# Kernel tuning notes

Hardware: AMD Instinct MI355X
Metric: run time of the kernel (lower is better)

Reference implementation:

```python
import jax, jax.numpy as jnp
import numpy as np

N_HEAD, D_MODEL, D_K, D_V = 16, 1024, 64, 64
B, S = 4, 2048


def setup_inputs() -> dict:
    key = jax.random.key(0)
    ks = jax.random.split(key, 11)
    s = 0.02
    return {
        "q": jax.random.normal(ks[0], (B, S, D_MODEL), jnp.float32),
        "k": jax.random.normal(ks[1], (B, S, D_MODEL), jnp.float32),
        "v": jax.random.normal(ks[2], (B, S, D_MODEL), jnp.float32),
        "Wq": jax.random.normal(ks[3], (D_MODEL, N_HEAD * D_K), jnp.float32) * s,
        "bq": jnp.zeros((N_HEAD * D_K,), jnp.float32),
        "Wk": jax.random.normal(ks[4], (D_MODEL, N_HEAD * D_K), jnp.float32) * s,
        "bk": jnp.zeros((N_HEAD * D_K,), jnp.float32),
        "Wv": jax.random.normal(ks[5], (D_MODEL, N_HEAD * D_V), jnp.float32) * s,
        "bv": jnp.zeros((N_HEAD * D_V,), jnp.float32),
        "Wo": jax.random.normal(ks[6], (N_HEAD * D_V, D_MODEL), jnp.float32) * s,
        "bo": jnp.zeros((D_MODEL,), jnp.float32),
    }


def reference(q, k, v, Wq, bq, Wk, bk, Wv, bv, Wo, bo):
    b, s, _ = q.shape
    # project and split heads: [B,S,H,Dk] -> [B,H,S,Dk]
    qh = (q @ Wq + bq).reshape(b, s, N_HEAD, D_K).transpose(0, 2, 1, 3)
    kh = (k @ Wk + bk).reshape(b, s, N_HEAD, D_K).transpose(0, 2, 1, 3)
    vh = (v @ Wv + bv).reshape(b, s, N_HEAD, D_V).transpose(0, 2, 1, 3)
    scale = 1.0 / jnp.sqrt(jnp.float32(D_K))
    scores = jnp.einsum("bhqd,bhkd->bhqk", qh, kh) * scale  # [B,H,S,S]
    atten = jax.nn.softmax(scores, axis=-1)
    out = jnp.einsum("bhqk,bhkd->bhqd", atten, vh)  # [B,H,S,Dv]
    out = out.transpose(0, 2, 1, 3).reshape(b, s, N_HEAD * D_V)
    return out @ Wo + bo
```

## Files before the change

### kernel.cpp

```cpp
#include <hip/hip_runtime.h>

typedef unsigned short u16;
typedef __attribute__((ext_vector_type(4))) float f32x4;
typedef __attribute__((ext_vector_type(16))) float f32x16;
typedef __attribute__((ext_vector_type(8))) short bf16x8;
typedef __attribute__((ext_vector_type(4))) u16 u16x4;
typedef __attribute__((ext_vector_type(8))) u16 u16x8;

#define MFMA16(a, b, c) __builtin_amdgcn_mfma_f32_16x16x32_bf16((a), (b), (c), 0, 0, 0)
#define MFMA32(a, b, c) __builtin_amdgcn_mfma_f32_32x32x16_bf16((a), (b), (c), 0, 0, 0)

__device__ __forceinline__ u16 f2bf(float f) {
  union { float f; unsigned u; } x; x.f = f;
  unsigned r = x.u + 0x7fffu + ((x.u >> 16) & 1u);
  return (u16)(r >> 16);
}

__device__ __forceinline__ unsigned cvtpk(float lo, float hi) {
  unsigned r;
  asm("v_cvt_pk_bf16_f32 %0, %1, %2" : "=v"(r) : "v"(lo), "v"(hi));
  return r;
}

__device__ __forceinline__ void gl_lds16(const void* g, void* l) {
  __builtin_amdgcn_global_load_lds((const __attribute__((address_space(1))) void*)g,
                                   (__attribute__((address_space(3))) void*)l,
                                   16, 0, 0);
}

__global__ __launch_bounds__(256) void cvt3_k(const float* __restrict__ q, const float* __restrict__ k,
                                              const float* __restrict__ v, u16* __restrict__ dst, int n4) {
  const float* src = blockIdx.y == 0 ? q : (blockIdx.y == 1 ? k : v);
  u16* d = dst + (size_t)blockIdx.y * 8192 * 1024;
  int idx = blockIdx.x * blockDim.x + threadIdx.x;
  int stride = gridDim.x * blockDim.x;
  for (int i = idx; i < n4; i += stride) {
    float4 vv = ((const float4*)src)[i];
    u16x4 o;
    o[0] = f2bf(vv.x); o[1] = f2bf(vv.y); o[2] = f2bf(vv.z); o[3] = f2bf(vv.w);
    ((u16x4*)d)[i] = o;
  }
}

__global__ __launch_bounds__(256) void cvtT_k(const float* __restrict__ W0, const float* __restrict__ W1,
                                              const float* __restrict__ W2, const float* __restrict__ W3,
                                              u16* __restrict__ T0, u16* __restrict__ T1,
                                              u16* __restrict__ T2, u16* __restrict__ T3) {
  __shared__ u16 t[64][72];
  const float* W; u16* T;
  switch (blockIdx.z) {
    case 0: W = W0; T = T0; break;
    case 1: W = W1; T = T1; break;
    case 2: W = W2; T = T2; break;
    default: W = W3; T = T3; break;
  }
  const int tid = threadIdx.x;
  const int tr = blockIdx.x, tc = blockIdx.y;
#pragma unroll
  for (int i = 0; i < 4; ++i) {
    int row = i * 16 + (tid >> 4);
    int c4 = tid & 15;
    float4 v = *(const float4*)&W[(size_t)(tr * 64 + row) * 1024 + tc * 64 + c4 * 4];
    t[row][c4 * 4 + 0] = f2bf(v.x);
    t[row][c4 * 4 + 1] = f2bf(v.y);
    t[row][c4 * 4 + 2] = f2bf(v.z);
    t[row][c4 * 4 + 3] = f2bf(v.w);
  }
  __syncthreads();
#pragma unroll
  for (int i = 0; i < 4; ++i) {
    int orow = i * 16 + (tid >> 4);
    int occ = tid & 15;
    u16x4 o;
#pragma unroll
    for (int j = 0; j < 4; ++j) o[j] = t[occ * 4 + j][orow];
    *(u16x4*)&T[(size_t)(tc * 64 + orow) * 1024 + tr * 64 + occ * 4] = o;
  }
}

__global__ __launch_bounds__(256) void gemm_qkv_k(const u16* __restrict__ Xb, const u16* __restrict__ WTb,
                                                  const float* __restrict__ bq, const float* __restrict__ bk,
                                                  const float* __restrict__ bv,
                                                  u16* __restrict__ Qh, u16* __restrict__ Kh,
                                                  u16* __restrict__ Vt, float qscale) {
  __shared__ u16 As[128 * 64];
  __shared__ u16 Bs[128 * 64];
  const int tid = threadIdx.x;
  const int lane = tid & 63;
  const int w = tid >> 6;
  const int which = blockIdx.y >> 3;
  const int m0 = blockIdx.x * 128;
  const int n0 = (blockIdx.y & 7) * 128;
  const u16* X = Xb + (size_t)which * 8192 * 1024;
  const u16* WT = WTb + (size_t)which * 1024 * 1024;
  const float* bias = which == 0 ? bq : (which == 1 ? bk : bv);
  const int wr = (w >> 1) * 64;
  const int wc = (w & 1) * 64;
  const int srow = lane >> 3;
  const int sch = (lane & 7) * 8;
  f32x4 acc[4][4] = {};

  for (int ks = 0; ks < 16; ++ks) {
    const int k0 = ks * 64;
#pragma unroll
    for (int i = 0; i < 4; ++i) {
      int row = i * 32 + w * 8 + srow;
      gl_lds16(X + (size_t)(m0 + row) * 1024 + k0 + sch, &As[(i * 32 + w * 8) * 64]);
      gl_lds16(WT + (size_t)(n0 + row) * 1024 + k0 + sch, &Bs[(i * 32 + w * 8) * 64]);
    }
    __syncthreads();
#pragma unroll
    for (int kk = 0; kk < 2; ++kk) {
      bf16x8 a[4], b[4];
#pragma unroll
      for (int t = 0; t < 4; ++t) {
        a[t] = *(const bf16x8*)&As[(wr + t * 16 + (lane & 15)) * 64 + kk * 32 + (lane >> 4) * 8];
        b[t] = *(const bf16x8*)&Bs[(wc + t * 16 + (lane & 15)) * 64 + kk * 32 + (lane >> 4) * 8];
      }
#pragma unroll
      for (int mi = 0; mi < 4; ++mi)
#pragma unroll
        for (int ni = 0; ni < 4; ++ni)
          acc[mi][ni] = MFMA16(a[mi], b[ni], acc[mi][ni]);
    }
    __syncthreads();
  }

  const int lr = (lane >> 4) * 4;
  const int lc = lane & 15;
  if (which <= 1) {
    u16* ob = which == 0 ? Qh : Kh;
    float scale = which == 0 ? qscale : 1.0f;
#pragma unroll
    for (int mi = 0; mi < 4; ++mi)
#pragma unroll
      for (int ni = 0; ni < 4; ++ni) {
        int n = n0 + wc + ni * 16 + lc;
        float bb = bias[n];
        int h = n >> 6, d = n & 63;
#pragma unroll
        for (int r = 0; r < 4; ++r) {
          int m = m0 + wr + mi * 16 + lr + r;
          int b = m >> 11, s = m & 2047;
          ob[(((size_t)(b * 16 + h) * 2048 + s) << 6) + d] = f2bf((acc[mi][ni][r] + bb) * scale);
        }
      }
  } else {
#pragma unroll
    for (int mi = 0; mi < 4; ++mi)
#pragma unroll
      for (int ni = 0; ni < 4; ++ni) {
        int n = n0 + wc + ni * 16 + lc;
        float bb = bias[n];
        int h = n >> 6, d = n & 63;
        int m = m0 + wr + mi * 16 + lr;
        int b = m >> 11, s = m & 2047;
        u16x4 pk;
#pragma unroll
        for (int r = 0; r < 4; ++r) pk[r] = f2bf(acc[mi][ni][r] + bb);
        *(u16x4*)&Vt[((size_t)(b * 16 + h) * 64 + d) * 2048 + s] = pk;
      }
  }
}

__global__ __launch_bounds__(256) void gemm_o_k(const u16* __restrict__ X, const u16* __restrict__ WT,
                                                const float* __restrict__ bias, float* __restrict__ out) {
  __shared__ u16 As[128 * 64];
  __shared__ u16 Bs[128 * 64];
  const int tid = threadIdx.x;
  const int lane = tid & 63;
  const int w = tid >> 6;
  const int m0 = blockIdx.x * 128;
  const int n0 = blockIdx.y * 128;
  const int wr = (w >> 1) * 64;
  const int wc = (w & 1) * 64;
  const int srow = lane >> 3;
  const int sch = (lane & 7) * 8;
  f32x4 acc[4][4] = {};

  for (int ks = 0; ks < 16; ++ks) {
    const int k0 = ks * 64;
#pragma unroll
    for (int i = 0; i < 4; ++i) {
      int row = i * 32 + w * 8 + srow;
      gl_lds16(X + (size_t)(m0 + row) * 1024 + k0 + sch, &As[(i * 32 + w * 8) * 64]);
      gl_lds16(WT + (size_t)(n0 + row) * 1024 + k0 + sch, &Bs[(i * 32 + w * 8) * 64]);
    }
    __syncthreads();
#pragma unroll
    for (int kk = 0; kk < 2; ++kk) {
      bf16x8 a[4], b[4];
#pragma unroll
      for (int t = 0; t < 4; ++t) {
        a[t] = *(const bf16x8*)&As[(wr + t * 16 + (lane & 15)) * 64 + kk * 32 + (lane >> 4) * 8];
        b[t] = *(const bf16x8*)&Bs[(wc + t * 16 + (lane & 15)) * 64 + kk * 32 + (lane >> 4) * 8];
      }
#pragma unroll
      for (int mi = 0; mi < 4; ++mi)
#pragma unroll
        for (int ni = 0; ni < 4; ++ni)
          acc[mi][ni] = MFMA16(a[mi], b[ni], acc[mi][ni]);
    }
    __syncthreads();
  }

  const int lr = (lane >> 4) * 4;
  const int lc = lane & 15;
#pragma unroll
  for (int mi = 0; mi < 4; ++mi)
#pragma unroll
    for (int ni = 0; ni < 4; ++ni) {
      int n = n0 + wc + ni * 16 + lc;
      float bb = bias[n];
#pragma unroll
      for (int r = 0; r < 4; ++r) {
        int m = m0 + wr + mi * 16 + lr + r;
        out[(size_t)m * 1024 + n] = acc[mi][ni][r] + bb;
      }
    }
}

__global__ __launch_bounds__(512) void attn_k(const u16* __restrict__ Qh, const u16* __restrict__ Kh,
                                              const u16* __restrict__ Vt, u16* __restrict__ AO) {
  __shared__ u16 SMEM[6 * 4096];
  u16* KL = SMEM;
  u16* VL = SMEM + 3 * 4096;
  const int lane = threadIdx.x & 63, w = threadIdx.x >> 6;
  const int hi = lane >> 5, q = lane & 31;

  const int id = blockIdx.x;
  const int bh = ((id >> 3) & 7) * 8 + (id & 7);
  const int qt = id >> 6;
  const int q0 = qt * 256 + w * 32;

  const u16* Qb = Qh + (size_t)bh * 2048 * 64;
  const u16* Kb = Kh + (size_t)bh * 2048 * 64;
  const u16* Vb = Vt + (size_t)bh * 64 * 2048;

  bf16x8 qf[4];
#pragma unroll
  for (int c = 0; c < 4; ++c)
    qf[c] = *(const bf16x8*)&Qb[(size_t)(q0 + q) * 64 + c * 16 + hi * 8];

  f32x16 o0 = {}, o1 = {};
  float l_ = 0.f;

  const int skh = (w & 1) * 32;
  const int sck = ((w >> 1) * 2 + hi) * 8;
  const int srowK = skh + q;
  const int lo8 = lane * 8;

#define STAGE(buf_, kt_) do {                                                   \
    int k0_ = (kt_) * 64;                                                       \
    gl_lds16(Kb + (size_t)(k0_ + srowK) * 64 + sck, &KL[(buf_) * 4096 + w * 512]); \
    gl_lds16(Vb + (size_t)srowK * 2048 + k0_ + sck, &VL[(buf_) * 4096 + w * 512]); \
  } while (0)

  STAGE(0, 0);
  STAGE(1, 1);
  STAGE(2, 2);

  for (int kt = 0; kt < 32; ++kt) {
    if (kt < 30) asm volatile("s_waitcnt vmcnt(4)" ::: "memory");
    else         asm volatile("s_waitcnt vmcnt(0)" ::: "memory");
    __builtin_amdgcn_s_barrier();
    __builtin_amdgcn_sched_barrier(0);

    const u16* Kc = &KL[(kt % 3) * 4096];
    const u16* Vc = &VL[(kt % 3) * 4096];

    f32x16 s0 = {}, s1 = {};
    __builtin_amdgcn_s_setprio(1);
#pragma unroll
    for (int c = 0; c < 4; ++c) {
      bf16x8 k0 = *(const bf16x8*)&Kc[(c * 2) * 512 + lo8];
      bf16x8 k1 = *(const bf16x8*)&Kc[(c * 2 + 1) * 512 + lo8];
      s0 = MFMA32(k0, qf[c], s0);
      s1 = MFMA32(k1, qf[c], s1);
    }
    __builtin_amdgcn_s_setprio(0);

#pragma unroll
    for (int i = 0; i < 16; ++i) {
      s0[i] = __builtin_exp2f(s0[i]);
      s1[i] = __builtin_exp2f(s1[i]);
    }
    float sum = 0.f;
#pragma unroll
    for (int i = 0; i < 16; ++i) sum += s0[i] + s1[i];
    l_ += sum;

    __builtin_amdgcn_s_setprio(1);
#pragma unroll
    for (int t = 0; t < 4; ++t) {
      unsigned wA, wB, wC, wD;
      if (t == 0) { wA = cvtpk(s0[0], s0[1]); wB = cvtpk(s0[2], s0[3]); wC = cvtpk(s0[4], s0[5]); wD = cvtpk(s0[6], s0[7]); }
      else if (t == 1) { wA = cvtpk(s0[8], s0[9]); wB = cvtpk(s0[10], s0[11]); wC = cvtpk(s0[12], s0[13]); wD = cvtpk(s0[14], s0[15]); }
      else if (t == 2) { wA = cvtpk(s1[0], s1[1]); wB = cvtpk(s1[2], s1[3]); wC = cvtpk(s1[4], s1[5]); wD = cvtpk(s1[6], s1[7]); }
      else { wA = cvtpk(s1[8], s1[9]); wB = cvtpk(s1[10], s1[11]); wC = cvtpk(s1[12], s1[13]); wD = cvtpk(s1[14], s1[15]); }
      asm("v_permlane32_swap_b32 %0, %1" : "+v"(wA), "+v"(wC));
      asm("v_permlane32_swap_b32 %0, %1" : "+v"(wB), "+v"(wD));
      union { unsigned u[4]; bf16x8 v; } pf;
      pf.u[0] = wA; pf.u[1] = wB; pf.u[2] = wC; pf.u[3] = wD;
      bf16x8 v0 = *(const bf16x8*)&Vc[(t * 2) * 512 + lo8];
      bf16x8 v1 = *(const bf16x8*)&Vc[(t * 2 + 1) * 512 + lo8];
      o0 = MFMA32(v0, pf.v, o0);
      o1 = MFMA32(v1, pf.v, o1);
    }
    __builtin_amdgcn_s_setprio(0);

    __builtin_amdgcn_sched_barrier(0);
    __builtin_amdgcn_s_barrier();
    if (kt < 29) STAGE(kt % 3, kt + 3);
  }
#undef STAGE

  l_ += __shfl_xor(l_, 32);
  u16* ep = SMEM + w * 2048;
  float inv = 1.0f / l_;
#pragma unroll
  for (int g = 0; g < 2; ++g) {
    const f32x16 oo = g ? o1 : o0;
#pragma unroll
    for (int j = 0; j < 8; ++j) {
      int d = g * 32 + (j & 1) * 2 + ((j >> 1) & 1) * 8 + (j >> 2) * 16 + 4 * hi;
      unsigned pw = cvtpk(oo[2 * j] * inv, oo[2 * j + 1] * inv);
      *(unsigned*)&ep[q * 64 + ((d >> 3) ^ (q & 7)) * 8 + (d & 7)] = pw;
    }
  }
  asm volatile("s_waitcnt lgkmcnt(0)" ::: "memory");
  const int b = bh >> 4, h = bh & 15;
#pragma unroll
  for (int i = 0; i < 4; ++i) {
    int r = i * 8 + (lane >> 3), c = lane & 7;
    u16x8 vv = *(const u16x8*)&ep[r * 64 + ((c ^ (r & 7)) * 8)];
    size_t row = (size_t)b * 2048 + q0 + r;
    *(u16x8*)&AO[row * 1024 + h * 64 + c * 8] = vv;
  }
}

extern "C" void kernel_launch(void* const* d_in, const int* in_sizes, int n_in,
                              void* d_out, int out_size, void* d_ws, size_t ws_size,
                              hipStream_t stream) {
  const float* q  = (const float*)d_in[0];
  const float* k  = (const float*)d_in[1];
  const float* v  = (const float*)d_in[2];
  const float* Wq = (const float*)d_in[3];
  const float* bq = (const float*)d_in[4];
  const float* Wk = (const float*)d_in[5];
  const float* bk = (const float*)d_in[6];
  const float* Wv = (const float*)d_in[7];
  const float* bv = (const float*)d_in[8];
  const float* Wo = (const float*)d_in[9];
  const float* bo = (const float*)d_in[10];
  float* out = (float*)d_out;

  char* ws = (char*)d_ws;
  const size_t SZX = (size_t)8192 * 1024 * 2;
  const size_t SZW = (size_t)1024 * 1024 * 2;
  u16* Xq  = (u16*)(ws);
  u16* WTq = (u16*)(ws + 3 * SZX);
  u16* WTk = (u16*)(ws + 3 * SZX + SZW);
  u16* WTv = (u16*)(ws + 3 * SZX + 2 * SZW);
  u16* WTo = (u16*)(ws + 3 * SZX + 3 * SZW);
  u16* Qh  = (u16*)(ws + 3 * SZX + 4 * SZW);
  u16* Kh  = (u16*)(ws + 4 * SZX + 4 * SZW);
  u16* Vt  = (u16*)(ws + 5 * SZX + 4 * SZW);
  u16* AO  = Xq;

  const int n4 = 8192 * 1024 / 4;
  cvt3_k<<<dim3(1024, 3), dim3(256), 0, stream>>>(q, k, v, Xq, n4);
  cvtT_k<<<dim3(16, 16, 4), dim3(256), 0, stream>>>(Wq, Wk, Wv, Wo, WTq, WTk, WTv, WTo);

  gemm_qkv_k<<<dim3(64, 24), dim3(256), 0, stream>>>(Xq, WTq, bq, bk, bv, Qh, Kh, Vt,
                                                     0.125f * 1.4426950408889634f);

  attn_k<<<dim3(512), dim3(512), 0, stream>>>(Qh, Kh, Vt, AO);

  gemm_o_k<<<dim3(64, 8), dim3(256), 0, stream>>>(AO, WTo, bo, out);
}
```

Before: 227.8 us.

## Double-buffer 128-key tiles with one barrier per tile in attention

Replaces the triple-buffered 64-key K/V LDS pipeline with a double-buffered 128-key tile. Each iteration now waits for all loads, passes a single barrier, then issues the next tile's prefetch before computing. This halves the number of loop iterations and removes the second barrier per tile. It also swaps the block-to-(batch,head) index mapping, which changes L2 locality across blocks. The cost is less prefetch depth (vmcnt(0) every tile) and a larger LDS footprint of 64KB.

```diff
diff --git a/kernel.cpp b/kernel.cpp
--- a/kernel.cpp
+++ b/kernel.cpp
@@ -222,14 +222,12 @@
 
 __global__ __launch_bounds__(512) void attn_k(const u16* __restrict__ Qh, const u16* __restrict__ Kh,
                                               const u16* __restrict__ Vt, u16* __restrict__ AO) {
-  __shared__ u16 SMEM[6 * 4096];
-  u16* KL = SMEM;
-  u16* VL = SMEM + 3 * 4096;
+  __shared__ u16 SMEM[2 * 16384];
   const int lane = threadIdx.x & 63, w = threadIdx.x >> 6;
   const int hi = lane >> 5, q = lane & 31;
 
   const int id = blockIdx.x;
-  const int bh = ((id >> 3) & 7) * 8 + (id & 7);
+  const int bh = (id & 7) * 8 + ((id >> 3) & 7);
   const int qt = id >> 6;
   const int q0 = qt * 256 + w * 32;
 
@@ -244,76 +242,78 @@
 
   f32x16 o0 = {}, o1 = {};
   float l_ = 0.f;
-
-  const int skh = (w & 1) * 32;
-  const int sck = ((w >> 1) * 2 + hi) * 8;
-  const int srowK = skh + q;
   const int lo8 = lane * 8;
 
-#define STAGE(buf_, kt_) do {                                                   \
-    int k0_ = (kt_) * 64;                                                       \
-    gl_lds16(Kb + (size_t)(k0_ + srowK) * 64 + sck, &KL[(buf_) * 4096 + w * 512]); \
-    gl_lds16(Vb + (size_t)srowK * 2048 + k0_ + sck, &VL[(buf_) * 4096 + w * 512]); \
+#define STAGE(slot_, kt_) do {                                                        \
+    int k0_ = (kt_) * 128;                                                            \
+    u16* KS_ = SMEM + (slot_) * 16384;                                                \
+    u16* VS_ = KS_ + 8192;                                                            \
+    _Pragma("unroll")                                                                 \
+    for (int j_ = 0; j_ < 2; ++j_) {                                                  \
+      int f_ = 2 * w + j_;                                                            \
+      int kh_ = f_ >> 2, c_ = f_ & 3;                                                 \
+      gl_lds16(Kb + (size_t)(k0_ + kh_ * 32 + q) * 64 + (c_ * 2 + hi) * 8, KS_ + f_ * 512); \
+      gl_lds16(Vb + (size_t)(j_ * 32 + q) * 2048 + k0_ + (w * 2 + hi) * 8, VS_ + (w * 2 + j_) * 512); \
+    }                                                                                 \
   } while (0)
 
   STAGE(0, 0);
-  STAGE(1, 1);
-  STAGE(2, 2);
-
-  for (int kt = 0; kt < 32; ++kt) {
-    if (kt < 30) asm volatile("s_waitcnt vmcnt(4)" ::: "memory");
-    else         asm volatile("s_waitcnt vmcnt(0)" ::: "memory");
+
+  for (int kt = 0; kt < 16; ++kt) {
+    asm volatile("s_waitcnt vmcnt(0)" ::: "memory");
     __builtin_amdgcn_s_barrier();
+    if (kt < 15) STAGE((kt + 1) & 1, kt + 1);
     __builtin_amdgcn_sched_barrier(0);
 
-    const u16* Kc = &KL[(kt % 3) * 4096];
-    const u16* Vc = &VL[(kt % 3) * 4096];
-
-    f32x16 s0 = {}, s1 = {};
-    __builtin_amdgcn_s_setprio(1);
-#pragma unroll
-    for (int c = 0; c < 4; ++c) {
-      bf16x8 k0 = *(const bf16x8*)&Kc[(c * 2) * 512 + lo8];
-      bf16x8 k1 = *(const bf16x8*)&Kc[(c * 2 + 1) * 512 + lo8];
-      s0 = MFMA32(k0, qf[c], s0);
-      s1 = MFMA32(k1, qf[c], s1);
-    }
-    __builtin_amdgcn_s_setprio(0);
-
-#pragma unroll
-    for (int i = 0; i < 16; ++i) {
-      s0[i] = __builtin_exp2f(s0[i]);
-      s1[i] = __builtin_exp2f(s1[i]);
-    }
-    float sum = 0.f;
-#pragma unroll
-    for (int i = 0; i < 16; ++i) sum += s0[i] + s1[i];
-    l_ += sum;
-
-    __builtin_amdgcn_s_setprio(1);
-#pragma unroll
-    for (int t = 0; t < 4; ++t) {
-      unsigned wA, wB, wC, wD;
-      if (t == 0) { wA = cvtpk(s0[0], s0[1]); wB = cvtpk(s0[2], s0[3]); wC = cvtpk(s0[4], s0[5]); wD = cvtpk(s0[6], s0[7]); }
-      else if (t == 1) { wA = cvtpk(s0[8], s0[9]); wB = cvtpk(s0[10], s0[11]); wC = cvtpk(s0[12], s0[13]); wD = cvtpk(s0[14], s0[15]); }
-      else if (t == 2) { wA = cvtpk(s1[0], s1[1]); wB = cvtpk(s1[2], s1[3]); wC = cvtpk(s1[4], s1[5]); wD = cvtpk(s1[6], s1[7]); }
-      else { wA = cvtpk(s1[8], s1[9]); wB = cvtpk(s1[10], s1[11]); wC = cvtpk(s1[12], s1[13]); wD = cvtpk(s1[14], s1[15]); }
-      asm("v_permlane32_swap_b32 %0, %1" : "+v"(wA), "+v"(wC));
-      asm("v_permlane32_swap_b32 %0, %1" : "+v"(wB), "+v"(wD));
-      union { unsigned u[4]; bf16x8 v; } pf;
-      pf.u[0] = wA; pf.u[1] = wB; pf.u[2] = wC; pf.u[3] = wD;
-      bf16x8 v0 = *(const bf16x8*)&Vc[(t * 2) * 512 + lo8];
-      bf16x8 v1 = *(const bf16x8*)&Vc[(t * 2 + 1) * 512 + lo8];
-      o0 = MFMA32(v0, pf.v, o0);
-      o1 = MFMA32(v1, pf.v, o1);
-    }
-    __builtin_amdgcn_s_setprio(0);
-
-    __builtin_amdgcn_sched_barrier(0);
-    __builtin_amdgcn_s_barrier();
-    if (kt < 29) STAGE(kt % 3, kt + 3);
+    const u16* KS = SMEM + (kt & 1) * 16384;
+    const u16* VS = KS + 8192;
+
+#pragma unroll
+    for (int r = 0; r < 2; ++r) {
+      f32x16 s0 = {}, s1 = {};
+      __builtin_amdgcn_s_setprio(1);
+#pragma unroll
+      for (int c = 0; c < 4; ++c) {
+        bf16x8 k0 = *(const bf16x8*)&KS[((2 * r) * 4 + c) * 512 + lo8];
+        bf16x8 k1 = *(const bf16x8*)&KS[((2 * r + 1) * 4 + c) * 512 + lo8];
+        s0 = MFMA32(k0, qf[c], s0);
+        s1 = MFMA32(k1, qf[c], s1);
+      }
+      __builtin_amdgcn_s_setprio(0);
+
+#pragma unroll
+      for (int i = 0; i < 16; ++i) {
+        s0[i] = __builtin_exp2f(s0[i]);
+        s1[i] = __builtin_exp2f(s1[i]);
+      }
+      float sum = 0.f;
+#pragma unroll
+      for (int i = 0; i < 16; ++i) sum += s0[i] + s1[i];
+      l_ += sum;
+
+      __builtin_amdgcn_s_setprio(1);
+#pragma unroll
+      for (int t = 0; t < 4; ++t) {
+        unsigned wA, wB, wC, wD;
+        if (t == 0) { wA = cvtpk(s0[0], s0[1]); wB = cvtpk(s0[2], s0[3]); wC = cvtpk(s0[4], s0[5]); wD = cvtpk(s0[6], s0[7]); }
+        else if (t == 1) { wA = cvtpk(s0[8], s0[9]); wB = cvtpk(s0[10], s0[11]); wC = cvtpk(s0[12], s0[13]); wD = cvtpk(s0[14], s0[15]); }
+        else if (t == 2) { wA = cvtpk(s1[0], s1[1]); wB = cvtpk(s1[2], s1[3]); wC = cvtpk(s1[4], s1[5]); wD = cvtpk(s1[6], s1[7]); }
+        else { wA = cvtpk(s1[8], s1[9]); wB = cvtpk(s1[10], s1[11]); wC = cvtpk(s1[12], s1[13]); wD = cvtpk(s1[14], s1[15]); }
+        asm("v_permlane32_swap_b32 %0, %1" : "+v"(wA), "+v"(wC));
+        asm("v_permlane32_swap_b32 %0, %1" : "+v"(wB), "+v"(wD));
+        union { unsigned u[4]; bf16x8 v; } pf;
+        pf.u[0] = wA; pf.u[1] = wB; pf.u[2] = wC; pf.u[3] = wD;
+        bf16x8 v0 = *(const bf16x8*)&VS[((4 * r + t) * 2) * 512 + lo8];
+        bf16x8 v1 = *(const bf16x8*)&VS[((4 * r + t) * 2 + 1) * 512 + lo8];
+        o0 = MFMA32(v0, pf.v, o0);
+        o1 = MFMA32(v1, pf.v, o1);
+      }
+      __builtin_amdgcn_s_setprio(0);
+    }
   }
 #undef STAGE
+
+  __builtin_amdgcn_s_barrier();
 
   l_ += __shfl_xor(l_, 32);
   u16* ep = SMEM + w * 2048;
```

Result: slower. 238.5 us (+4.7%).

## Use four-slot LDS ring to drop second barrier, compute rowsum via MFMA

Applied to the files above, without the earlier changes.

The attention loop now uses a four-slot LDS ring instead of three, so the next tile can be issued right after the single per-iteration barrier. This removes the trailing barrier and lets the prefetch overlap the current tile's compute. The softmax denominator is now computed by an extra MFMA against a ones vector on the bf16 probabilities, replacing the scalar VALU sum and the cross-lane shuffle. The cost is 64KB of LDS instead of 48KB, one more MFMA per tile, and a denominator built from bf16-rounded probabilities.

```diff
diff --git a/kernel.cpp b/kernel.cpp
--- a/kernel.cpp
+++ b/kernel.cpp
@@ -222,9 +222,7 @@
 
 __global__ __launch_bounds__(512) void attn_k(const u16* __restrict__ Qh, const u16* __restrict__ Kh,
                                               const u16* __restrict__ Vt, u16* __restrict__ AO) {
-  __shared__ u16 SMEM[6 * 4096];
-  u16* KL = SMEM;
-  u16* VL = SMEM + 3 * 4096;
+  __shared__ u16 SMEM[4 * 8192];
   const int lane = threadIdx.x & 63, w = threadIdx.x >> 6;
   const int hi = lane >> 5, q = lane & 31;
 
@@ -242,18 +240,20 @@
   for (int c = 0; c < 4; ++c)
     qf[c] = *(const bf16x8*)&Qb[(size_t)(q0 + q) * 64 + c * 16 + hi * 8];
 
-  f32x16 o0 = {}, o1 = {};
-  float l_ = 0.f;
-
-  const int skh = (w & 1) * 32;
+  bf16x8 onesf;
+#pragma unroll
+  for (int i = 0; i < 8; ++i) onesf[i] = (short)0x3F80;
+
+  f32x16 o0 = {}, o1 = {}, ol = {};
+  const int lo8 = lane * 8;
+
+  const int srowK = (w & 1) * 32 + q;
   const int sck = ((w >> 1) * 2 + hi) * 8;
-  const int srowK = skh + q;
-  const int lo8 = lane * 8;
-
-#define STAGE(buf_, kt_) do {                                                   \
-    int k0_ = (kt_) * 64;                                                       \
-    gl_lds16(Kb + (size_t)(k0_ + srowK) * 64 + sck, &KL[(buf_) * 4096 + w * 512]); \
-    gl_lds16(Vb + (size_t)srowK * 2048 + k0_ + sck, &VL[(buf_) * 4096 + w * 512]); \
+
+#define STAGE(slot_, kt_) do {                                                       \
+    int k0_ = (kt_) * 64;                                                            \
+    gl_lds16(Kb + (size_t)(k0_ + srowK) * 64 + sck, &SMEM[(slot_) * 8192 + w * 512]);          \
+    gl_lds16(Vb + (size_t)srowK * 2048 + k0_ + sck, &SMEM[(slot_) * 8192 + 4096 + w * 512]);   \
   } while (0)
 
   STAGE(0, 0);
@@ -261,13 +261,15 @@
   STAGE(2, 2);
 
   for (int kt = 0; kt < 32; ++kt) {
-    if (kt < 30) asm volatile("s_waitcnt vmcnt(4)" ::: "memory");
-    else         asm volatile("s_waitcnt vmcnt(0)" ::: "memory");
+    if (kt < 30)       asm volatile("s_waitcnt vmcnt(4)" ::: "memory");
+    else if (kt == 30) asm volatile("s_waitcnt vmcnt(2)" ::: "memory");
+    else               asm volatile("s_waitcnt vmcnt(0)" ::: "memory");
     __builtin_amdgcn_s_barrier();
+    if (kt <= 28) STAGE((kt + 3) & 3, kt + 3);
     __builtin_amdgcn_sched_barrier(0);
 
-    const u16* Kc = &KL[(kt % 3) * 4096];
-    const u16* Vc = &VL[(kt % 3) * 4096];
+    const u16* Kc = &SMEM[(kt & 3) * 8192];
+    const u16* Vc = Kc + 4096;
 
     f32x16 s0 = {}, s1 = {};
     __builtin_amdgcn_s_setprio(1);
@@ -285,10 +287,6 @@
       s0[i] = __builtin_exp2f(s0[i]);
       s1[i] = __builtin_exp2f(s1[i]);
     }
-    float sum = 0.f;
-#pragma unroll
-    for (int i = 0; i < 16; ++i) sum += s0[i] + s1[i];
-    l_ += sum;
 
     __builtin_amdgcn_s_setprio(1);
 #pragma unroll
@@ -306,18 +304,16 @@
       bf16x8 v1 = *(const bf16x8*)&Vc[(t * 2 + 1) * 512 + lo8];
       o0 = MFMA32(v0, pf.v, o0);
       o1 = MFMA32(v1, pf.v, o1);
+      ol = MFMA32(onesf, pf.v, ol);
     }
     __builtin_amdgcn_s_setprio(0);
-
-    __builtin_amdgcn_sched_barrier(0);
-    __builtin_amdgcn_s_barrier();
-    if (kt < 29) STAGE(kt % 3, kt + 3);
   }
 #undef STAGE
 
-  l_ += __shfl_xor(l_, 32);
+  __builtin_amdgcn_s_barrier();
+
+  float inv = 1.0f / ol[0];
   u16* ep = SMEM + w * 2048;
-  float inv = 1.0f / l_;
 #pragma unroll
   for (int g = 0; g < 2; ++g) {
     const f32x16 oo = g ? o1 : o0;
```

Measured after the change: 227.4 us. Within noise of the previous version (-0.2%).
